# Performance work log

Hardware: AMD Instinct MI355X
Metric: run time of the kernel (lower is better)

## Reference

```python
import jax, jax.numpy as jnp
import numpy as np

MARGIN = 2.0   # self.m
SCALE = 30.0   # cosine-head logit scale


def setup_inputs() -> dict:
    key = jax.random.key(0)
    k1, k2, k3 = jax.random.split(key, 3)
    B, D, C = 8192, 256, 5994
    emb = jax.random.normal(k1, (B, D), dtype=jnp.float32)
    W = jax.random.normal(k2, (C, D), dtype=jnp.float32) * 0.05
    y = jax.random.randint(k3, (B,), 0, C, dtype=jnp.int32)
    # first half domain 0 (main), second half domain 1 (target)
    y_d = jnp.concatenate([jnp.zeros(B // 2, jnp.int32), jnp.ones(B // 2, jnp.int32)])
    return {"emb": emb, "W": W, "y": y, "y_d": y_d}


def _clf_head(emb, W, y):
    # cosine-similarity classifier + cross-entropy (standard ASV clf head)
    e = emb / (jnp.linalg.norm(emb, axis=1, keepdims=True) + 1e-12)
    w = W / (jnp.linalg.norm(W, axis=1, keepdims=True) + 1e-12)
    logits = SCALE * (e @ w.T)                     # [B, C]
    logp = jax.nn.log_softmax(logits, axis=-1)
    loss = -jnp.mean(jnp.take_along_axis(logp, y[:, None], axis=1))
    acc = jnp.mean((jnp.argmax(logits, axis=-1) == y).astype(jnp.float32))
    return loss, acc


def reference(emb, W, y, y_d):
    B, D = emb.shape
    H = B // 2
    idx = jnp.arange(B)
    # faithful scatter: domain-0 rows -> main_emb[i]; domain-1 rows -> target_emb[i % H]
    # out-of-range sentinel H is dropped (rows with wrong domain stay zero)
    main_idx = jnp.where(y_d == 0, idx, H)
    tgt_idx = jnp.where(y_d != 0, idx % H, H)
    main_emb = jnp.zeros((H, D), emb.dtype).at[main_idx].set(emb, mode="drop")
    target_emb = jnp.zeros((H, D), emb.dtype).at[tgt_idx].set(emb, mode="drop")

    loss_c, acc = _clf_head(emb, W, y)

    # pairwise diffs: even rows main[i]-main[(i+1)%H] (label 1), odd rows main[i]-target[i] (label 0)
    pos_diff = main_emb - jnp.roll(main_emb, -1, axis=0)  # [H, D]
    neg_diff = main_emb - target_emb                      # [H, D]
    das_diff = jnp.stack([pos_diff, neg_diff], axis=1).reshape(B, D)
    das_label = jnp.tile(jnp.array([1.0, 0.0], emb.dtype), H)  # [B]

    das_dist = jnp.linalg.norm(das_diff, axis=1)
    das_loss = jnp.mean((1.0 - das_label) * das_dist ** 2
                        + das_label * jnp.maximum(MARGIN - das_dist, 0.0) ** 2)
    das_dist_mean = jnp.mean(jax.lax.stop_gradient(das_dist))
    return (loss_c, das_loss, acc, das_dist_mean)
```

## Files before the change

### kernel.cpp

```cpp
#include <hip/hip_runtime.h>
#include <hip/hip_bf16.h>

#define B_ROWS 8192
#define DIM 256
#define C_CLS 5994
#define N_CHUNK 188
#define NSPL 8
#define H_HALF 4096
#define SCALE_F 30.0f
#define MAXL 30.0f
#define EXPC 43.2808512266689f

#if defined(__has_builtin)
#if __has_builtin(__builtin_amdgcn_exp2f)
#define EXP2(x) __builtin_amdgcn_exp2f(x)
#endif
#endif
#ifndef EXP2
#define EXP2(x) exp2f(x)
#endif

typedef _Float16 half8 __attribute__((ext_vector_type(8)));
typedef float f32x16 __attribute__((ext_vector_type(16)));

__global__ __launch_bounds__(256)
void k_pack(const float* __restrict__ emb, const float* __restrict__ W,
            _Float16* __restrict__ en_blk, _Float16* __restrict__ wn_blk,
            float* __restrict__ rne, float* __restrict__ rnw,
            float* __restrict__ accum) {
  __shared__ float ssm[256];
  __shared__ float rnl[32];
  const int b = blockIdx.x;
  const int t = threadIdx.x;
  if (b == 0 && t < 8) accum[t] = 0.f;
  const bool isW = b >= (B_ROWS/32);
  const int tile = isW ? b - (B_ROWS/32) : b;
  const int l31 = t & 31;
  const int row = tile*32 + l31;
  const float* __restrict__ src = isW ? W : emb;
  const bool rv = (!isW) || (row < C_CLS);

  float v[4][8];
  float ss = 0.f;
  #pragma unroll
  for (int i=0;i<4;i++) {
    const int d0 = ((t>>6) + i*4)*16 + ((t>>5)&1)*8;
    if (rv) {
      float4 x0 = *(const float4*)(src + (size_t)row*DIM + d0);
      float4 x1 = *(const float4*)(src + (size_t)row*DIM + d0 + 4);
      v[i][0]=x0.x; v[i][1]=x0.y; v[i][2]=x0.z; v[i][3]=x0.w;
      v[i][4]=x1.x; v[i][5]=x1.y; v[i][6]=x1.z; v[i][7]=x1.w;
      ss += x0.x*x0.x + x0.y*x0.y + x0.z*x0.z + x0.w*x0.w
          + x1.x*x1.x + x1.y*x1.y + x1.z*x1.z + x1.w*x1.w;
    } else {
      #pragma unroll
      for (int j=0;j<8;j++) v[i][j] = 0.f;
    }
  }
  ssm[t] = ss;
  __syncthreads();
  if (t < 32) {
    float s = 0.f;
    #pragma unroll
    for (int j=0;j<8;j++) s += ssm[t + j*32];
    float rn = 1.0f/(sqrtf(s) + 1e-12f);
    rnl[t] = rn;
    int rw = tile*32 + t;
    if (!isW) rne[rw] = rn;
    else if (rw < C_CLS) rnw[rw] = rn;
  }
  __syncthreads();
  const float rn = rnl[l31];
  _Float16* __restrict__ dst = (isW ? wn_blk : en_blk) + (size_t)tile*8192;
  #pragma unroll
  for (int i=0;i<4;i++) {
    half8 h;
    #pragma unroll
    for (int j=0;j<8;j++) h[j] = (_Float16)(v[i][j]*rn);
    *(half8*)(dst + t*8 + i*2048) = h;
  }
}

__global__ __launch_bounds__(256, 2)
void k_logits(const _Float16* __restrict__ en_blk, const _Float16* __restrict__ wn_blk,
              float* __restrict__ psum, unsigned* __restrict__ pkey) {
  const int split = blockIdx.x & (NSPL-1);
  const int panel = blockIdx.x / NSPL;
  const int wid  = threadIdx.x >> 6;
  const int lane = threadIdx.x & 63;
  const int l31  = lane & 31;
  const int lh   = lane >> 5;
  const int tile = panel*4 + wid;

  half8 a[16];
  const _Float16* ab = en_blk + (size_t)tile*8192 + lane*8;
  #pragma unroll
  for (int k=0;k<16;k++) a[k] = *(const half8*)(ab + k*512);

  float ssum[16]; unsigned key[16];
  #pragma unroll
  for (int r=0;r<16;r++){ ssum[r]=0.f; key[r]=0u; }

  const int nit = (N_CHUNK - split + NSPL - 1) / NSPL;
  const _Float16* p = wn_blk + (size_t)split*8192 + lane*8;
  const ptrdiff_t STEP = (ptrdiff_t)NSPL*8192;

  half8 b0[8], b1[8];
  #pragma unroll
  for (int k=0;k<8;k++) b0[k] = *(const half8*)(p + k*512);
  #pragma unroll
  for (int k=0;k<8;k++) b1[k] = *(const half8*)(p + (k+8)*512);

  unsigned colu = (unsigned)(split*32 + l31);
  for (int it = 0; it < nit-1; ++it) {
    const _Float16* pn = p + STEP;
    f32x16 acc = {};
    #pragma unroll
    for (int k=0;k<8;k++)
      acc = __builtin_amdgcn_mfma_f32_32x32x16_f16(a[k], b0[k], acc, 0,0,0);
    #pragma unroll
    for (int k=0;k<8;k++) b0[k] = *(const half8*)(pn + k*512);
    #pragma unroll
    for (int k=0;k<8;k++)
      acc = __builtin_amdgcn_mfma_f32_32x32x16_f16(a[k+8], b1[k], acc, 0,0,0);
    #pragma unroll
    for (int k=0;k<8;k++) b1[k] = *(const half8*)(pn + (k+8)*512);
    #pragma unroll
    for (int r=0;r<16;r++) {
      float x = acc[r];
      ssum[r] += EXP2(fmaf(x, EXPC, -EXPC));
      unsigned ky = (__float_as_uint(x + 2.0f) & 0xFFFFE000u) | colu;
      key[r] = ky > key[r] ? ky : key[r];
    }
    colu += NSPL*32;
    p = pn;
  }
  {
    f32x16 acc = {};
    #pragma unroll
    for (int k=0;k<8;k++)
      acc = __builtin_amdgcn_mfma_f32_32x32x16_f16(a[k], b0[k], acc, 0,0,0);
    #pragma unroll
    for (int k=0;k<8;k++)
      acc = __builtin_amdgcn_mfma_f32_32x32x16_f16(a[k+8], b1[k], acc, 0,0,0);
    #pragma unroll
    for (int r=0;r<16;r++) {
      float x = acc[r];
      ssum[r] += EXP2(fmaf(x, EXPC, -EXPC));
      unsigned ky = (__float_as_uint(x + 2.0f) & 0xFFFFE000u) | colu;
      key[r] = ky > key[r] ? ky : key[r];
    }
  }

  #pragma unroll
  for (int off=1; off<32; off<<=1) {
    #pragma unroll
    for (int r=0;r<16;r++) {
      ssum[r] += __shfl_xor(ssum[r], off);
      unsigned o = __shfl_xor(key[r], off);
      key[r] = o > key[r] ? o : key[r];
    }
  }
  if (l31 == 0) {
    const int rowbase = tile*32;
    #pragma unroll
    for (int r=0;r<16;r++) {
      int row = rowbase + (r&3) + 8*(r>>2) + 4*lh;
      psum[split*B_ROWS + row] = ssum[r];
      pkey[split*B_ROWS + row] = key[r];
    }
  }
}

__global__ __launch_bounds__(256)
void k_tail(const float* __restrict__ emb, const float* __restrict__ W,
            const int* __restrict__ y, const int* __restrict__ y_d,
            const float* __restrict__ rne, const float* __restrict__ rnw,
            const float* __restrict__ psum, const unsigned* __restrict__ pkey,
            float* __restrict__ accum, float* __restrict__ out) {
  __shared__ float s0[4], s1[4];
  const int wid = threadIdx.x >> 6, lane = threadIdx.x & 63;
  if (blockIdx.x < 128) {
    float lacc = 0.f, cacc = 0.f;
    for (int row = blockIdx.x*4 + wid; row < B_ROWS; row += 512) {
      const int yc = y[row];
      float4 e = *(const float4*)(emb + (size_t)row*DIM + lane*4);
      float4 w = *(const float4*)(W + (size_t)yc*DIM + lane*4);
      float d = e.x*w.x + e.y*w.y + e.z*w.z + e.w*w.w;
      #pragma unroll
      for (int off=1; off<64; off<<=1) d += __shfl_xor(d, off);
      float S = 0.f; unsigned km = 0u;
      if (lane < NSPL) {
        S = psum[lane*B_ROWS + row];
        km = pkey[lane*B_ROWS + row];
      }
      #pragma unroll
      for (int off=1; off<NSPL; off<<=1) {
        S += __shfl_xor(S, off);
        unsigned o = __shfl_xor(km, off);
        if (o > km) km = o;
      }
      if (lane == 0) {
        float ly = SCALE_F * d * rne[row] * rnw[yc];
        lacc += MAXL + logf(S) - ly;
        cacc += ((km & 0x1FFFu) == (unsigned)yc) ? 1.f : 0.f;
      }
    }
    if (lane == 0) { s0[wid] = lacc; s1[wid] = cacc; }
    __syncthreads();
    if (threadIdx.x == 0) {
      atomicAdd(&accum[0], s0[0]+s0[1]+s0[2]+s0[3]);
      atomicAdd(&accum[1], s1[0]+s1[1]+s1[2]+s1[3]);
    }
  } else {
    float a2 = 0.f, a3 = 0.f;
    for (int i = (blockIdx.x-128)*4 + wid; i < H_HALF; i += 256) {
      const int j = (i+1) & (H_HALF-1);
      const int di = y_d[i], dj = y_d[j], dih = y_d[i + H_HALF];
      float4 z = {0.f,0.f,0.f,0.f};
      float4 mi = (di==0)  ? *(const float4*)(emb + (size_t)i*DIM + lane*4) : z;
      float4 mj = (dj==0)  ? *(const float4*)(emb + (size_t)j*DIM + lane*4) : z;
      float4 ti = (dih!=0) ? *(const float4*)(emb + (size_t)(i+H_HALF)*DIM + lane*4)
                           : ((di!=0) ? *(const float4*)(emb + (size_t)i*DIM + lane*4) : z);
      float px = mi.x-mj.x, py = mi.y-mj.y, pz = mi.z-mj.z, pw = mi.w-mj.w;
      float nx = mi.x-ti.x, ny = mi.y-ti.y, nz = mi.z-ti.z, nw = mi.w-ti.w;
      float sp = px*px+py*py+pz*pz+pw*pw;
      float sn = nx*nx+ny*ny+nz*nz+nw*nw;
      #pragma unroll
      for (int off=1; off<64; off<<=1) { sp += __shfl_xor(sp, off); sn += __shfl_xor(sn, off); }
      if (lane == 0) {
        float dp = sqrtf(sp), dn = sqrtf(sn);
        float m = fmaxf(2.0f - dp, 0.f);
        a2 += m*m + dn*dn;
        a3 += dp + dn;
      }
    }
    if (lane == 0) { s0[wid] = a2; s1[wid] = a3; }
    __syncthreads();
    if (threadIdx.x == 0) {
      atomicAdd(&accum[2], s0[0]+s0[1]+s0[2]+s0[3]);
      atomicAdd(&accum[3], s1[0]+s1[1]+s1[2]+s1[3]);
    }
  }
  if (threadIdx.x == 0) {
    __threadfence();
    unsigned* cnt = (unsigned*)(accum + 4);
    unsigned done = atomicAdd(cnt, 1u);
    if (done == 191u) {
      float v0 = atomicAdd(&accum[0], 0.f);
      float v1 = atomicAdd(&accum[1], 0.f);
      float v2 = atomicAdd(&accum[2], 0.f);
      float v3 = atomicAdd(&accum[3], 0.f);
      out[0] = v0 * (1.0f/B_ROWS);
      out[1] = v2 * (1.0f/B_ROWS);
      out[2] = v1 * (1.0f/B_ROWS);
      out[3] = v3 * (1.0f/B_ROWS);
    }
  }
}

extern "C" void kernel_launch(void* const* d_in, const int* in_sizes, int n_in,
                              void* d_out, int out_size, void* d_ws, size_t ws_size,
                              hipStream_t stream) {
  const float* emb = (const float*)d_in[0];
  const float* W   = (const float*)d_in[1];
  const int*   y   = (const int*)d_in[2];
  const int*   y_d = (const int*)d_in[3];

  char* ws = (char*)d_ws;
  const size_t EN_OFF   = 0;
  const size_t WN_OFF   = EN_OFF  + (size_t)256*16384;
  const size_t RNE_OFF  = WN_OFF  + (size_t)N_CHUNK*16384;
  const size_t RNW_OFF  = RNE_OFF + (size_t)B_ROWS*4;
  const size_t PSUM_OFF = RNW_OFF + 24064;
  const size_t PKEY_OFF = PSUM_OFF + (size_t)NSPL*B_ROWS*4;
  const size_t ACC_OFF  = PKEY_OFF + (size_t)NSPL*B_ROWS*4;

  _Float16* en_blk = (_Float16*)(ws + EN_OFF);
  _Float16* wn_blk = (_Float16*)(ws + WN_OFF);
  float*    rne   = (float*)(ws + RNE_OFF);
  float*    rnw   = (float*)(ws + RNW_OFF);
  float*    psum  = (float*)(ws + PSUM_OFF);
  unsigned* pkey  = (unsigned*)(ws + PKEY_OFF);
  float*    accum = (float*)(ws + ACC_OFF);

  k_pack<<<B_ROWS/32 + N_CHUNK, 256, 0, stream>>>(emb, W, en_blk, wn_blk, rne, rnw, accum);
  k_logits<<<64*NSPL, 256, 0, stream>>>(en_blk, wn_blk, psum, pkey);
  k_tail<<<192, 256, 0, stream>>>(emb, W, y, y_d, rne, rnw, psum, pkey, accum, (float*)d_out);
}
```

Baseline: 76.37 us.

## Compute two 32-row A tiles per wave to reuse each W fragment

Each wave now holds two 32-row blocks of normalized embeddings and issues two independent MFMA chains against every loaded W fragment, halving W traffic per output and interleaving independent accumulators. The grid is halved to 256 blocks and launch bounds drop to one block per SIMD group, since register use roughly doubles. This lowers occupancy and leaves only 256 blocks on a 256-CU part, so latency hiding now depends on the two-chain ILP rather than on extra waves.

New measurement: 80.79 us. 5.8% more time.

```diff
diff --git a/kernel.cpp b/kernel.cpp
--- a/kernel.cpp
+++ b/kernel.cpp
@@ -81,7 +81,7 @@
   }
 }
 
-__global__ __launch_bounds__(256, 2)
+__global__ __launch_bounds__(256, 1)
 void k_logits(const _Float16* __restrict__ en_blk, const _Float16* __restrict__ wn_blk,
               float* __restrict__ psum, unsigned* __restrict__ pkey) {
   const int split = blockIdx.x & (NSPL-1);
@@ -90,16 +90,20 @@
   const int lane = threadIdx.x & 63;
   const int l31  = lane & 31;
   const int lh   = lane >> 5;
-  const int tile = panel*4 + wid;
-
-  half8 a[16];
-  const _Float16* ab = en_blk + (size_t)tile*8192 + lane*8;
-  #pragma unroll
-  for (int k=0;k<16;k++) a[k] = *(const half8*)(ab + k*512);
-
-  float ssum[16]; unsigned key[16];
-  #pragma unroll
-  for (int r=0;r<16;r++){ ssum[r]=0.f; key[r]=0u; }
+  const int t64  = panel*4 + wid;
+
+  half8 a0[16], a1[16];
+  {
+    const _Float16* ab = en_blk + (size_t)t64*16384 + lane*8;
+    #pragma unroll
+    for (int k=0;k<16;k++) a0[k] = *(const half8*)(ab + k*512);
+    #pragma unroll
+    for (int k=0;k<16;k++) a1[k] = *(const half8*)(ab + 8192 + k*512);
+  }
+
+  float ssum0[16], ssum1[16]; unsigned key0[16], key1[16];
+  #pragma unroll
+  for (int r=0;r<16;r++){ ssum0[r]=0.f; key0[r]=0u; ssum1[r]=0.f; key1[r]=0u; }
 
   const int nit = (N_CHUNK - split + NSPL - 1) / NSPL;
   const _Float16* p = wn_blk + (size_t)split*8192 + lane*8;
@@ -114,41 +118,57 @@
   unsigned colu = (unsigned)(split*32 + l31);
   for (int it = 0; it < nit-1; ++it) {
     const _Float16* pn = p + STEP;
-    f32x16 acc = {};
-    #pragma unroll
-    for (int k=0;k<8;k++)
-      acc = __builtin_amdgcn_mfma_f32_32x32x16_f16(a[k], b0[k], acc, 0,0,0);
+    f32x16 acc0 = {}, acc1 = {};
+    #pragma unroll
+    for (int k=0;k<8;k++) {
+      acc0 = __builtin_amdgcn_mfma_f32_32x32x16_f16(a0[k], b0[k], acc0, 0,0,0);
+      acc1 = __builtin_amdgcn_mfma_f32_32x32x16_f16(a1[k], b0[k], acc1, 0,0,0);
+    }
     #pragma unroll
     for (int k=0;k<8;k++) b0[k] = *(const half8*)(pn + k*512);
     #pragma unroll
-    for (int k=0;k<8;k++)
-      acc = __builtin_amdgcn_mfma_f32_32x32x16_f16(a[k+8], b1[k], acc, 0,0,0);
+    for (int k=0;k<8;k++) {
+      acc0 = __builtin_amdgcn_mfma_f32_32x32x16_f16(a0[k+8], b1[k], acc0, 0,0,0);
+      acc1 = __builtin_amdgcn_mfma_f32_32x32x16_f16(a1[k+8], b1[k], acc1, 0,0,0);
+    }
     #pragma unroll
     for (int k=0;k<8;k++) b1[k] = *(const half8*)(pn + (k+8)*512);
     #pragma unroll
     for (int r=0;r<16;r++) {
-      float x = acc[r];
-      ssum[r] += EXP2(fmaf(x, EXPC, -EXPC));
+      float x = acc0[r];
+      ssum0[r] += EXP2(fmaf(x, EXPC, -EXPC));
       unsigned ky = (__float_as_uint(x + 2.0f) & 0xFFFFE000u) | colu;
-      key[r] = ky > key[r] ? ky : key[r];
+      key0[r] = ky > key0[r] ? ky : key0[r];
+      float x1 = acc1[r];
+      ssum1[r] += EXP2(fmaf(x1, EXPC, -EXPC));
+      unsigned ky1 = (__float_as_uint(x1 + 2.0f) & 0xFFFFE000u) | colu;
+      key1[r] = ky1 > key1[r] ? ky1 : key1[r];
     }
     colu += NSPL*32;
     p = pn;
   }
   {
-    f32x16 acc = {};
-    #pragma unroll
-    for (int k=0;k<8;k++)
-      acc = __builtin_amdgcn_mfma_f32_32x32x16_f16(a[k], b0[k], acc, 0,0,0);
-    #pragma unroll
-    for (int k=0;k<8;k++)
-      acc = __builtin_amdgcn_mfma_f32_32x32x16_f16(a[k+8], b1[k], acc, 0,0,0);
+    f32x16 acc0 = {}, acc1 = {};
+    #pragma unroll
+    for (int k=0;k<8;k++) {
+      acc0 = __builtin_amdgcn_mfma_f32_32x32x16_f16(a0[k], b0[k], acc0, 0,0,0);
+      acc1 = __builtin_amdgcn_mfma_f32_32x32x16_f16(a1[k], b0[k], acc1, 0,0,0);
+    }
+    #pragma unroll
+    for (int k=0;k<8;k++) {
+      acc0 = __builtin_amdgcn_mfma_f32_32x32x16_f16(a0[k+8], b1[k], acc0, 0,0,0);
+      acc1 = __builtin_amdgcn_mfma_f32_32x32x16_f16(a1[k+8], b1[k], acc1, 0,0,0);
+    }
     #pragma unroll
     for (int r=0;r<16;r++) {
-      float x = acc[r];
-      ssum[r] += EXP2(fmaf(x, EXPC, -EXPC));
+      float x = acc0[r];
+      ssum0[r] += EXP2(fmaf(x, EXPC, -EXPC));
       unsigned ky = (__float_as_uint(x + 2.0f) & 0xFFFFE000u) | colu;
-      key[r] = ky > key[r] ? ky : key[r];
+      key0[r] = ky > key0[r] ? ky : key0[r];
+      float x1 = acc1[r];
+      ssum1[r] += EXP2(fmaf(x1, EXPC, -EXPC));
+      unsigned ky1 = (__float_as_uint(x1 + 2.0f) & 0xFFFFE000u) | colu;
+      key1[r] = ky1 > key1[r] ? ky1 : key1[r];
     }
   }
 
@@ -156,18 +176,23 @@
   for (int off=1; off<32; off<<=1) {
     #pragma unroll
     for (int r=0;r<16;r++) {
-      ssum[r] += __shfl_xor(ssum[r], off);
-      unsigned o = __shfl_xor(key[r], off);
-      key[r] = o > key[r] ? o : key[r];
+      ssum0[r] += __shfl_xor(ssum0[r], off);
+      unsigned o0 = __shfl_xor(key0[r], off);
+      key0[r] = o0 > key0[r] ? o0 : key0[r];
+      ssum1[r] += __shfl_xor(ssum1[r], off);
+      unsigned o1 = __shfl_xor(key1[r], off);
+      key1[r] = o1 > key1[r] ? o1 : key1[r];
     }
   }
   if (l31 == 0) {
-    const int rowbase = tile*32;
+    const int rowbase = t64*64;
     #pragma unroll
     for (int r=0;r<16;r++) {
-      int row = rowbase + (r&3) + 8*(r>>2) + 4*lh;
-      psum[split*B_ROWS + row] = ssum[r];
-      pkey[split*B_ROWS + row] = key[r];
+      int rr = (r&3) + 8*(r>>2) + 4*lh;
+      psum[split*B_ROWS + rowbase + rr] = ssum0[r];
+      pkey[split*B_ROWS + rowbase + rr] = key0[r];
+      psum[split*B_ROWS + rowbase + 32 + rr] = ssum1[r];
+      pkey[split*B_ROWS + rowbase + 32 + rr] = key1[r];
     }
   }
 }
@@ -285,6 +310,6 @@
   float*    accum = (float*)(ws + ACC_OFF);
 
   k_pack<<<B_ROWS/32 + N_CHUNK, 256, 0, stream>>>(emb, W, en_blk, wn_blk, rne, rnw, accum);
-  k_logits<<<64*NSPL, 256, 0, stream>>>(en_blk, wn_blk, psum, pkey);
+  k_logits<<<32*NSPL, 256, 0, stream>>>(en_blk, wn_blk, psum, pkey);
   k_tail<<<192, 256, 0, stream>>>(emb, W, y, y_d, rne, rnw, psum, pkey, accum, (float*)d_out);
 }
```
